# Kernel tuning notes

Measured on AMD Instinct MI355X. Metric: run time of the kernel, lower is better.

Reference implementation:

```python
import jax, jax.numpy as jnp
import numpy as np

B, N, DF, DC = 16, 4096, 128, 3
N_GROUP, K_GROUP = 1024, 16
D_IN, D_OUT = DC + DF, 256  # d_features = [131, 256]
BN_EPS = 1e-5


def farthest_point_sample(coord, n_sample):
    # coord: [B, N, 3] -> idx: [B, n_sample] (deterministic start at point 0)
    b, n, _ = coord.shape
    dist0 = jnp.full((b, n), jnp.inf, coord.dtype)
    idx0 = jnp.zeros((b,), jnp.int32)

    def step(carry, _):
        dist, last = carry
        last_pt = jnp.take_along_axis(coord, last[:, None, None].astype(jnp.int32), axis=1)  # [B,1,3]
        d = jnp.sum((coord - last_pt) ** 2, axis=-1)  # [B,N]
        dist = jnp.minimum(dist, d)
        nxt = jnp.argmax(dist, axis=1).astype(jnp.int32)
        return (dist, nxt), last

    _, idxs = jax.lax.scan(step, (dist0, idx0), None, length=n_sample)
    return jnp.swapaxes(idxs, 0, 1)  # [B, n_sample]


def knn_points(coord, center_coord, k):
    # squared distances [B, G, N]; k nearest source points per center
    d2 = jnp.sum((center_coord[:, :, None, :] - coord[:, None, :, :]) ** 2, axis=-1)
    _, idx = jax.lax.top_k(-d2, k)  # [B, G, k]
    return idx.astype(jnp.int32)


def index_points(points, idx):
    # points: [B, N, C]; idx: [B, ...] -> [B, ..., C]
    b = points.shape[0]
    batch_idx = jnp.arange(b).reshape((b,) + (1,) * (idx.ndim - 1))
    return points[batch_idx, idx]


def setup_inputs() -> dict:
    key = jax.random.key(0)
    k1, k2, k3, k4 = jax.random.split(key, 4)
    feature = jax.random.normal(k1, (B, N, DF), dtype=jnp.float32)
    coord = jax.random.normal(k2, (B, N, DC), dtype=jnp.float32)
    W = jax.random.normal(k3, (D_OUT, D_IN), dtype=jnp.float32) * (1.0 / np.sqrt(D_IN))
    b = jax.random.normal(k4, (D_OUT,), dtype=jnp.float32) * 0.01
    gamma = jnp.ones((D_OUT,), dtype=jnp.float32)
    beta = jnp.zeros((D_OUT,), dtype=jnp.float32)
    return {"feature": feature, "coord": coord, "W": W, "b": b, "gamma": gamma, "beta": beta}


def reference(feature, coord, W, b, gamma, beta):
    # --- group ---
    center_idx = farthest_point_sample(coord, N_GROUP)            # [B,G]
    center_coord = index_points(coord, center_idx)                 # [B,G,3]
    neigh_idx = knn_points(coord, center_coord, K_GROUP)           # [B,G,K]
    neigh_coord = index_points(coord, neigh_idx) - center_coord[:, :, None]  # [B,G,K,3]
    neigh_feature = jnp.concatenate([neigh_coord, index_points(feature, neigh_idx)], axis=-1)  # [B,G,K,131]
    # --- 1x1 conv + BatchNorm (train-mode batch stats, biased var) + ReLU ---
    y = jnp.einsum('bgkc,oc->bgko', neigh_feature, W) + b          # [B,G,K,256]
    mean = jnp.mean(y, axis=(0, 1, 2))
    var = jnp.mean((y - mean) ** 2, axis=(0, 1, 2))
    y = (y - mean) * jax.lax.rsqrt(var + BN_EPS) * gamma + beta
    y = jax.nn.relu(y)
    # --- max over neighbors ---
    center_feature = jnp.max(y, axis=2)                            # [B,G,256]
    return center_feature, center_coord
```

## Files before the change

### kernel.cpp

```cpp
#include <hip/hip_runtime.h>
#include <stdint.h>

#define BATCH 16
#define NPTS 4096
#define DFEAT 128
#define NGRP 1024
#define KNNK 16
#define DOUT_CH 256
#define KPAD 160
#define APAD 168
#define NGROUPS (BATCH*NGRP)
#define MROWS (NGROUPS*KNNK)
#define NWORKERS 240
#define NCHUNKS (NGROUPS/8)
#define CHUNKS_PER_BATCH (NGRP/8)
#define OUT_FEAT_ELEMS (NGROUPS*DOUT_CH)
#define KNN_SLOTS 512
#define PROG_STRIDE 16

typedef __attribute__((ext_vector_type(8))) short s16x8;
typedef __attribute__((ext_vector_type(8))) __bf16 bf16x8;
typedef __attribute__((ext_vector_type(4))) float f32x4;

union V8U { s16x8 s; bf16x8 b; };

__device__ inline unsigned short f2bf(float f) {
  unsigned u = __float_as_uint(f);
  unsigned r = 0x7FFFu + ((u >> 16) & 1u);
  return (unsigned short)((u + r) >> 16);
}

__device__ inline float sqdist3(float ax, float ay, float az,
                                float bx, float by, float bz) {
  float dx = __fsub_rn(ax, bx);
  float dy = __fsub_rn(ay, by);
  float dz = __fsub_rn(az, bz);
  return __fadd_rn(__fadd_rn(__fmul_rn(dx, dx), __fmul_rn(dy, dy)), __fmul_rn(dz, dz));
}

__device__ inline unsigned long long u64max(unsigned long long a, unsigned long long b) {
  return a > b ? a : b;
}

template<int CTRL>
__device__ inline unsigned long long dpp_max_step(unsigned long long k) {
  unsigned hi = (unsigned)(k >> 32), lo = (unsigned)k;
  unsigned hi2 = (unsigned)__builtin_amdgcn_update_dpp(0, (int)hi, CTRL, 0xF, 0xF, true);
  unsigned lo2 = (unsigned)__builtin_amdgcn_update_dpp(0, (int)lo, CTRL, 0xF, 0xF, true);
  unsigned long long k2 = ((unsigned long long)hi2 << 32) | lo2;
  return k2 > k ? k2 : k;
}
__device__ inline unsigned long long wave_max_u64(unsigned long long k) {
  k = dpp_max_step<0xB1>(k);
  k = dpp_max_step<0x4E>(k);
  k = dpp_max_step<0x141>(k);
  k = dpp_max_step<0x140>(k);
  k = dpp_max_step<0x142>(k);
  k = dpp_max_step<0x143>(k);
  return k;
}

template<int CTRL>
__device__ inline unsigned long long dpp_min_step(unsigned long long k) {
  unsigned hi = (unsigned)(k >> 32), lo = (unsigned)k;
  unsigned hi2 = (unsigned)__builtin_amdgcn_update_dpp((int)hi, (int)hi, CTRL, 0xF, 0xF, false);
  unsigned lo2 = (unsigned)__builtin_amdgcn_update_dpp((int)lo, (int)lo, CTRL, 0xF, 0xF, false);
  unsigned long long k2 = ((unsigned long long)hi2 << 32) | lo2;
  return k2 < k ? k2 : k;
}
__device__ inline unsigned long long wave_min_u64(unsigned long long k) {
  k = dpp_min_step<0xB1>(k);
  k = dpp_min_step<0x4E>(k);
  k = dpp_min_step<0x141>(k);
  k = dpp_min_step<0x140>(k);
  k = dpp_min_step<0x142>(k);
  k = dpp_min_step<0x143>(k);
  return k;
}

struct FpsSh {
  float4 c4[NPTS];
  float ocb[NGRP * 3];
  unsigned long long slots[2][4];
};
struct WrkSh {
  float wd[4][NPTS];
  float svd[4][KNN_SLOTS];
  int   svi[4][KNN_SLOTS];
  unsigned short Abuf[2][16][APAD];
  int   nidx_s[8][KNNK];
  float cent_s[8][3];
};
union ShU { FpsSh f; WrkSh w; };

__global__ __launch_bounds__(256)
void fused_kernel(const float* __restrict__ feat, const float* __restrict__ coord,
                  const float* __restrict__ W, float* __restrict__ out_coord,
                  unsigned short* __restrict__ Wb,
                  float* __restrict__ psum, float* __restrict__ psumsq,
                  float* __restrict__ wmax, float* __restrict__ wmin,
                  int* __restrict__ progress, int* __restrict__ wb_ready)
{
  __shared__ ShU sh;
  const int tid = threadIdx.x;
  const int w = tid >> 6;
  const int lane = tid & 63;

  if (blockIdx.x < BATCH) {
    const int b = blockIdx.x;
    float4* c4 = sh.f.c4;
    float* ocb = sh.f.ocb;

    const float* g = coord + (size_t)b * NPTS * 3;
    for (int p = tid; p < NPTS; p += 256)
      c4[p] = make_float4(g[3 * p], g[3 * p + 1], g[3 * p + 2], 0.f);
    __syncthreads();

    float px[16], py[16], pz[16], dist[16];
    unsigned lokey[16];
    #pragma unroll
    for (int j = 0; j < 16; ++j) {
      int p = tid + 256 * j;
      float4 c = c4[p];
      px[j] = c.x; py[j] = c.y; pz[j] = c.z;
      dist[j] = __builtin_inff();
      lokey[j] = 0xFFFFFFFFu - (unsigned)p;
    }

    float lx = c4[0].x, ly = c4[0].y, lz = c4[0].z;
    if (tid == 0) { ocb[0] = lx; ocb[1] = ly; ocb[2] = lz; }

    float* oc = out_coord + (size_t)b * NGRP * 3;
    int pend = 0;

    for (int i = 1; i < NGRP; ++i) {
      const int par = i & 1;
      unsigned long long cand[16];
      #pragma unroll
      for (int j = 0; j < 16; ++j) {
        float d  = sqdist3(px[j], py[j], pz[j], lx, ly, lz);
        float nd = fminf(dist[j], d);
        dist[j] = nd;
        cand[j] = ((unsigned long long)__float_as_uint(nd) << 32) | lokey[j];
      }
      #pragma unroll
      for (int st = 8; st >= 1; st >>= 1)
        #pragma unroll
        for (int j = 0; j < st; ++j)
          cand[j] = u64max(cand[j], cand[j + st]);
      unsigned long long best = wave_max_u64(cand[0]);
      if (lane == 63) sh.f.slots[par][w] = best;
      __syncthreads();

      if (pend) {
        if (tid == 0) {
          __threadfence();
          __hip_atomic_store(&progress[b * PROG_STRIDE], pend, __ATOMIC_RELEASE, __HIP_MEMORY_SCOPE_AGENT);
        }
        pend = 0;
      }
      if ((i & 7) == 0) {
        if (tid < 24) oc[(i - 8) * 3 + tid] = ocb[(i - 8) * 3 + tid];
        pend = i;
      }

      unsigned long long s0 = u64max(sh.f.slots[par][0], sh.f.slots[par][1]);
      unsigned long long s1 = u64max(sh.f.slots[par][2], sh.f.slots[par][3]);
      unsigned long long f = u64max(s0, s1);
      int mi = (int)(0xFFFFFFFFu - (unsigned)(f & 0xFFFFFFFFull));

      float4 cw = c4[mi];
      lx = cw.x; ly = cw.y; lz = cw.z;
      if (tid < 3) ocb[3 * i + tid] = (tid == 0) ? cw.x : ((tid == 1) ? cw.y : cw.z);
    }

    __syncthreads();
    #pragma unroll
    for (int qq = 0; qq < 12; ++qq) oc[tid + 256 * qq] = ocb[tid + 256 * qq];
    __syncthreads();
    if (tid == 0) {
      __threadfence();
      __hip_atomic_store(&progress[b * PROG_STRIDE], NGRP, __ATOMIC_RELEASE, __HIP_MEMORY_SCOPE_AGENT);
    }
    return;
  }

  const int wi = blockIdx.x - BATCH;

  if (wi == 0) {
    for (int i = tid; i < DOUT_CH * KPAD; i += 256) {
      int n = i / KPAD;
      int k = i - n * KPAD;
      float v = 0.f;
      if (k < 128)      v = W[n * 131 + 3 + k];
      else if (k < 131) v = W[n * 131 + (k - 128)];
      Wb[i] = f2bf(v);
    }
    __syncthreads();
    if (tid == 0) {
      __threadfence();
      __hip_atomic_store(wb_ready, 1, __ATOMIC_RELEASE, __HIP_MEMORY_SCOPE_AGENT);
    }
  }
  if (tid == 0) {
    while (__hip_atomic_load(wb_ready, __ATOMIC_RELAXED, __HIP_MEMORY_SCOPE_AGENT) == 0)
      __builtin_amdgcn_s_sleep(1);
    __threadfence();
  }
  __syncthreads();

  const int lr = lane & 15, q = lane >> 4;

  V8U bfrag[4][5];
  #pragma unroll
  for (int nt = 0; nt < 4; ++nt)
    #pragma unroll
    for (int kt = 0; kt < 5; ++kt) {
      int n = w * 64 + nt * 16 + lr;
      bfrag[nt][kt].s = *(const s16x8*)(Wb + n * KPAD + kt * 32 + q * 8);
    }

  for (int i = tid; i < 2 * 16 * 32; i += 256) {
    int buf = i >> 9, rr = (i >> 5) & 15, cc = 128 + (i & 31);
    sh.w.Abuf[buf][rr][cc] = 0;
  }
  float sum1[4] = {0, 0, 0, 0}, sum2[4] = {0, 0, 0, 0};
  __syncthreads();

  for (int ord = wi; ord < NCHUNKS; ord += NWORKERS) {
    const int b  = ord & 15;
    const int lc = ord >> 4;
    const int need = lc * 8 + 8;

    if (tid == 0) {
      while (__hip_atomic_load(&progress[b * PROG_STRIDE], __ATOMIC_RELAXED, __HIP_MEMORY_SCOPE_AGENT) < need)
        __builtin_amdgcn_s_sleep(16);
      __threadfence();
    }
    __syncthreads();

    if (tid < 24) sh.w.cent_s[tid / 3][tid % 3] =
        out_coord[(size_t)b * NGRP * 3 + lc * 24 + tid];
    __syncthreads();

    const float* pc = coord + (size_t)b * NPTS * 3;
    for (int k2 = 0; k2 < 2; ++k2) {
      const int k8 = w * 2 + k2;
      const float cx = sh.w.cent_s[k8][0], cy = sh.w.cent_s[k8][1], cz = sh.w.cent_s[k8][2];
      float* wd  = sh.w.wd[w];
      float* wsd = sh.w.svd[w];
      int*   wsi = sh.w.svi[w];

      float m = __builtin_inff();
      for (int tt = 0; tt < 64; ++tt) {
        int p = tt * 64 + lane;
        float d = sqdist3(cx, cy, cz, pc[3 * p], pc[3 * p + 1], pc[3 * p + 2]);
        wd[p] = d;
        m = fminf(m, d);
      }
      unsigned mb = __float_as_uint(m);
      unsigned prefix = 0u;
      for (int bit = 30; bit >= 0; --bit) {
        unsigned trial = prefix | (1u << bit);
        if (__popcll(__ballot(mb < trial)) < 16) prefix = trial;
      }
      const unsigned T = prefix;

      int base = 0;
      unsigned long long ltmask = (1ull << lane) - 1ull;
      for (int tt = 0; tt < 64; ++tt) {
        int p = tt * 64 + lane;
        float d = wd[p];
        bool keep = (__float_as_uint(d) <= T);
        unsigned long long mk = __ballot(keep);
        if (keep) {
          int pos = base + __popcll(mk & ltmask);
          if (pos < KNN_SLOTS) { wsd[pos] = d; wsi[pos] = p; }
        }
        base += __popcll(mk);
      }
      int S = base < KNN_SLOTS ? base : KNN_SLOTS;

      float rsd[8];
      #pragma unroll
      for (int k = 0; k < 8; ++k) {
        int s = lane + 64 * k;
        rsd[k] = (s < S) ? wsd[s] : __builtin_inff();
      }
      for (int r = 0; r < KNNK; ++r) {
        unsigned long long key = 0xFFFFFFFFFFFFFFFFull;
        #pragma unroll
        for (int k = 0; k < 8; ++k) {
          unsigned long long kk = ((unsigned long long)__float_as_uint(rsd[k]) << 32)
                                | (unsigned)(lane + 64 * k);
          key = kk < key ? kk : key;
        }
        key = wave_min_u64(key);
        int bs = __builtin_amdgcn_readlane((int)(unsigned)(key & 0xFFFFFFFFull), 63);
        #pragma unroll
        for (int k = 0; k < 8; ++k)
          if (lane == (bs & 63) && k == (bs >> 6)) rsd[k] = __builtin_inff();
        if (lane == 0) sh.w.nidx_s[k8][r] = wsi[bs];
      }
    }
    __syncthreads();

    auto stage = [&](int gi, int buf) {
      int r = tid >> 4, c16 = tid & 15;
      int np = sh.w.nidx_s[gi][r];
      const float* fr = feat + ((size_t)(b * NPTS + np)) * DFEAT + c16 * 8;
      float4 f0 = ((const float4*)fr)[0];
      float4 f1 = ((const float4*)fr)[1];
      s16x8 v;
      v[0] = f2bf(f0.x); v[1] = f2bf(f0.y); v[2] = f2bf(f0.z); v[3] = f2bf(f0.w);
      v[4] = f2bf(f1.x); v[5] = f2bf(f1.y); v[6] = f2bf(f1.z); v[7] = f2bf(f1.w);
      *(s16x8*)&sh.w.Abuf[buf][r][c16 * 8] = v;
      if (tid < 16) {
        int np2 = sh.w.nidx_s[gi][tid];
        const float* p = coord + ((size_t)(b * NPTS + np2)) * 3;
        sh.w.Abuf[buf][tid][128] = f2bf(p[0] - sh.w.cent_s[gi][0]);
        sh.w.Abuf[buf][tid][129] = f2bf(p[1] - sh.w.cent_s[gi][1]);
        sh.w.Abuf[buf][tid][130] = f2bf(p[2] - sh.w.cent_s[gi][2]);
      }
    };

    stage(0, 0);
    __syncthreads();

    for (int gi = 0; gi < 8; ++gi) {
      int cur = gi & 1;
      if (gi < 7) stage(gi + 1, cur ^ 1);

      f32x4 acc[4];
      #pragma unroll
      for (int nt = 0; nt < 4; ++nt) acc[nt] = (f32x4)0.0f;
      #pragma unroll
      for (int kt = 0; kt < 5; ++kt) {
        V8U a;
        a.s = *(const s16x8*)&sh.w.Abuf[cur][lr][kt * 32 + q * 8];
        #pragma unroll
        for (int nt = 0; nt < 4; ++nt)
          acc[nt] = __builtin_amdgcn_mfma_f32_16x16x32_bf16(a.b, bfrag[nt][kt].b, acc[nt], 0, 0, 0);
      }
      int gidx = (b * CHUNKS_PER_BATCH + lc) * 8 + gi;
      #pragma unroll
      for (int nt = 0; nt < 4; ++nt) {
        float r0 = acc[nt][0], r1 = acc[nt][1], r2 = acc[nt][2], r3 = acc[nt][3];
        float mx = fmaxf(fmaxf(r0, r1), fmaxf(r2, r3));
        float mn = fminf(fminf(r0, r1), fminf(r2, r3));
        sum1[nt] += r0 + r1 + r2 + r3;
        sum2[nt] += r0 * r0 + r1 * r1 + r2 * r2 + r3 * r3;
        mx = fmaxf(mx, __shfl_xor(mx, 16)); mn = fminf(mn, __shfl_xor(mn, 16));
        mx = fmaxf(mx, __shfl_xor(mx, 32)); mn = fminf(mn, __shfl_xor(mn, 32));
        if (q == 0) {
          int col = w * 64 + nt * 16 + lr;
          wmax[(size_t)gidx * DOUT_CH + col] = mx;
          wmin[(size_t)gidx * DOUT_CH + col] = mn;
        }
      }
      __syncthreads();
    }
  }

  #pragma unroll
  for (int nt = 0; nt < 4; ++nt) {
    float s1 = sum1[nt], s2 = sum2[nt];
    s1 += __shfl_xor(s1, 16); s2 += __shfl_xor(s2, 16);
    s1 += __shfl_xor(s1, 32); s2 += __shfl_xor(s2, 32);
    if (q == 0) {
      int col = w * 64 + nt * 16 + lr;
      psum[(size_t)col * NWORKERS + wi]   = s1;
      psumsq[(size_t)col * NWORKERS + wi] = s2;
    }
  }
}

__global__ __launch_bounds__(256)
void stats_kernel(const float* __restrict__ psum, const float* __restrict__ psumsq,
                  const float* __restrict__ gamma, const float* __restrict__ beta,
                  float* __restrict__ sc, float* __restrict__ tc)
{
  const int c = blockIdx.x;
  const int tid = threadIdx.x, lane = tid & 63, w = tid >> 6;
  float s1 = 0.f, s2 = 0.f;
  for (int r = tid; r < NWORKERS; r += 256) {
    s1 += psum[(size_t)c * NWORKERS + r];
    s2 += psumsq[(size_t)c * NWORKERS + r];
  }
  #pragma unroll
  for (int off = 1; off < 64; off <<= 1) { s1 += __shfl_xor(s1, off); s2 += __shfl_xor(s2, off); }
  __shared__ float a1[4], a2[4];
  if (lane == 0) { a1[w] = s1; a2[w] = s2; }
  __syncthreads();
  if (tid == 0) {
    float S1 = a1[0] + a1[1] + a1[2] + a1[3];
    float S2 = a2[0] + a2[1] + a2[2] + a2[3];
    const float inv = 1.0f / (float)MROWS;
    float mean = S1 * inv;
    float var  = S2 * inv - mean * mean;
    float rs = rsqrtf(var + 1e-5f);
    float s = gamma[c] * rs;
    sc[c] = s;
    tc[c] = beta[c] - mean * s;
  }
}

__global__ __launch_bounds__(256)
void final_kernel(const float* __restrict__ wmax, const float* __restrict__ wmin,
                  const float* __restrict__ sc, const float* __restrict__ tc,
                  float* __restrict__ out)
{
  int i4 = blockIdx.x * 256 + threadIdx.x;
  int base = i4 * 4;
  int c = base & (DOUT_CH - 1);
  float4 mx = *(const float4*)(wmax + base);
  float4 mn = *(const float4*)(wmin + base);
  float4 sv = *(const float4*)(sc + c);
  float4 tv = *(const float4*)(tc + c);
  float4 o;
  o.x = fmaxf(fmaf(sv.x, (sv.x > 0.f ? mx.x : mn.x), tv.x), 0.f);
  o.y = fmaxf(fmaf(sv.y, (sv.y > 0.f ? mx.y : mn.y), tv.y), 0.f);
  o.z = fmaxf(fmaf(sv.z, (sv.z > 0.f ? mx.z : mn.z), tv.z), 0.f);
  o.w = fmaxf(fmaf(sv.w, (sv.w > 0.f ? mx.w : mn.w), tv.w), 0.f);
  *(float4*)(out + base) = o;
}

extern "C" void kernel_launch(void* const* d_in, const int* in_sizes, int n_in,
                              void* d_out, int out_size, void* d_ws, size_t ws_size,
                              hipStream_t stream)
{
  const float* feature = (const float*)d_in[0];
  const float* coord   = (const float*)d_in[1];
  const float* W       = (const float*)d_in[2];
  const float* gamma   = (const float*)d_in[4];
  const float* beta    = (const float*)d_in[5];
  float* out = (float*)d_out;
  float* out_coord = out + OUT_FEAT_ELEMS;

  char* ws = (char*)d_ws;
  int*            flags  = (int*)(ws + 0);
  unsigned short* Wb     = (unsigned short*)(ws + 4096);
  float*          psum   = (float*)(ws + (1 << 20));
  float*          psumsq = (float*)(ws + (2 << 20));
  float*          sc     = (float*)(ws + (3 << 20));
  float*          tc     = (float*)(ws + (3 << 20) + 4096);
  float*          wmax   = (float*)(ws + (8 << 20));
  float*          wmin   = (float*)(ws + (8 << 20) + (size_t)OUT_FEAT_ELEMS * 4);
  int* progress = flags;
  int* wb_ready = flags + BATCH * PROG_STRIDE;

  hipMemsetAsync(flags, 0, (BATCH * PROG_STRIDE + 16) * sizeof(int), stream);

  hipLaunchKernelGGL(fused_kernel, dim3(BATCH + NWORKERS), dim3(256), 0, stream,
                     feature, coord, W, out_coord, Wb,
                     psum, psumsq, wmax, wmin, progress, wb_ready);
  hipLaunchKernelGGL(stats_kernel, dim3(DOUT_CH), dim3(256), 0, stream,
                     psum, psumsq, gamma, beta, sc, tc);
  hipLaunchKernelGGL(final_kernel, dim3(OUT_FEAT_ELEMS / 1024), dim3(256), 0, stream,
                     wmax, wmin, sc, tc, out);
}
```

Baseline: 799.4 us.

## Pack FPS distance math, batch progress publishes, simplify stats reduction

The farthest-point-sampling loop now computes two points' distances at a time with packed v_pk_add/v_pk_mul f32 instructions, which halves VALU issue on the serial critical path. Center coordinates are published every 32 iterations instead of every 8, and the explicit threadfences before the release stores are dropped. The per-worker BN partial sums move to a worker-major layout so a single-block stats kernel can reduce them with coalesced loads. Less frequent publishing may make consumer blocks wait longer for centers, and removing the fences relies on release semantics alone.

Measured after the change: 855.0 us. 7.0% more time.

```diff
diff --git a/kernel.cpp b/kernel.cpp
--- a/kernel.cpp
+++ b/kernel.cpp
@@ -21,6 +21,7 @@
 typedef __attribute__((ext_vector_type(8))) short s16x8;
 typedef __attribute__((ext_vector_type(8))) __bf16 bf16x8;
 typedef __attribute__((ext_vector_type(4))) float f32x4;
+typedef __attribute__((ext_vector_type(2))) float f32x2;
 
 union V8U { s16x8 s; bf16x8 b; };
 
@@ -36,6 +37,22 @@
   float dy = __fsub_rn(ay, by);
   float dz = __fsub_rn(az, bz);
   return __fadd_rn(__fadd_rn(__fmul_rn(dx, dx), __fmul_rn(dy, dy)), __fmul_rn(dz, dz));
+}
+
+__device__ inline f32x2 pk_sub(f32x2 a, f32x2 b) {
+  f32x2 d;
+  asm("v_pk_add_f32 %0, %1, %2 neg_lo:[0,1] neg_hi:[0,1]" : "=v"(d) : "v"(a), "v"(b));
+  return d;
+}
+__device__ inline f32x2 pk_mul(f32x2 a, f32x2 b) {
+  f32x2 d;
+  asm("v_pk_mul_f32 %0, %1, %2" : "=v"(d) : "v"(a), "v"(b));
+  return d;
+}
+__device__ inline f32x2 pk_add(f32x2 a, f32x2 b) {
+  f32x2 d;
+  asm("v_pk_add_f32 %0, %1, %2" : "=v"(d) : "v"(a), "v"(b));
+  return d;
 }
 
 __device__ inline unsigned long long u64max(unsigned long long a, unsigned long long b) {
@@ -116,15 +133,19 @@
       c4[p] = make_float4(g[3 * p], g[3 * p + 1], g[3 * p + 2], 0.f);
     __syncthreads();
 
-    float px[16], py[16], pz[16], dist[16];
+    f32x2 px2[8], py2[8], pz2[8], dist2[8];
     unsigned lokey[16];
     #pragma unroll
-    for (int j = 0; j < 16; ++j) {
-      int p = tid + 256 * j;
-      float4 c = c4[p];
-      px[j] = c.x; py[j] = c.y; pz[j] = c.z;
-      dist[j] = __builtin_inff();
-      lokey[j] = 0xFFFFFFFFu - (unsigned)p;
+    for (int j = 0; j < 8; ++j) {
+      int p0 = tid + 256 * (2 * j);
+      int p1 = tid + 256 * (2 * j + 1);
+      float4 a = c4[p0], c = c4[p1];
+      px2[j] = (f32x2){a.x, c.x};
+      py2[j] = (f32x2){a.y, c.y};
+      pz2[j] = (f32x2){a.z, c.z};
+      dist2[j] = (f32x2){__builtin_inff(), __builtin_inff()};
+      lokey[2 * j]     = 0xFFFFFFFFu - (unsigned)p0;
+      lokey[2 * j + 1] = 0xFFFFFFFFu - (unsigned)p1;
     }
 
     float lx = c4[0].x, ly = c4[0].y, lz = c4[0].z;
@@ -135,13 +156,22 @@
 
     for (int i = 1; i < NGRP; ++i) {
       const int par = i & 1;
+      f32x2 l2x = (f32x2){lx, lx};
+      f32x2 l2y = (f32x2){ly, ly};
+      f32x2 l2z = (f32x2){lz, lz};
+
       unsigned long long cand[16];
       #pragma unroll
-      for (int j = 0; j < 16; ++j) {
-        float d  = sqdist3(px[j], py[j], pz[j], lx, ly, lz);
-        float nd = fminf(dist[j], d);
-        dist[j] = nd;
-        cand[j] = ((unsigned long long)__float_as_uint(nd) << 32) | lokey[j];
+      for (int j = 0; j < 8; ++j) {
+        f32x2 dx = pk_sub(px2[j], l2x);
+        f32x2 dy = pk_sub(py2[j], l2y);
+        f32x2 dz = pk_sub(pz2[j], l2z);
+        f32x2 s = pk_add(pk_add(pk_mul(dx, dx), pk_mul(dy, dy)), pk_mul(dz, dz));
+        float n0 = fminf(dist2[j].x, s.x);
+        float n1 = fminf(dist2[j].y, s.y);
+        dist2[j] = (f32x2){n0, n1};
+        cand[2 * j]     = ((unsigned long long)__float_as_uint(n0) << 32) | lokey[2 * j];
+        cand[2 * j + 1] = ((unsigned long long)__float_as_uint(n1) << 32) | lokey[2 * j + 1];
       }
       #pragma unroll
       for (int st = 8; st >= 1; st >>= 1)
@@ -153,14 +183,12 @@
       __syncthreads();
 
       if (pend) {
-        if (tid == 0) {
-          __threadfence();
+        if (tid == 0)
           __hip_atomic_store(&progress[b * PROG_STRIDE], pend, __ATOMIC_RELEASE, __HIP_MEMORY_SCOPE_AGENT);
-        }
         pend = 0;
       }
-      if ((i & 7) == 0) {
-        if (tid < 24) oc[(i - 8) * 3 + tid] = ocb[(i - 8) * 3 + tid];
+      if ((i & 31) == 0) {
+        if (tid < 96) oc[(i - 32) * 3 + tid] = ocb[(i - 32) * 3 + tid];
         pend = i;
       }
 
@@ -178,10 +206,8 @@
     #pragma unroll
     for (int qq = 0; qq < 12; ++qq) oc[tid + 256 * qq] = ocb[tid + 256 * qq];
     __syncthreads();
-    if (tid == 0) {
-      __threadfence();
+    if (tid == 0)
       __hip_atomic_store(&progress[b * PROG_STRIDE], NGRP, __ATOMIC_RELEASE, __HIP_MEMORY_SCOPE_AGENT);
-    }
     return;
   }
 
@@ -197,10 +223,8 @@
       Wb[i] = f2bf(v);
     }
     __syncthreads();
-    if (tid == 0) {
-      __threadfence();
+    if (tid == 0)
       __hip_atomic_store(wb_ready, 1, __ATOMIC_RELEASE, __HIP_MEMORY_SCOPE_AGENT);
-    }
   }
   if (tid == 0) {
     while (__hip_atomic_load(wb_ready, __ATOMIC_RELAXED, __HIP_MEMORY_SCOPE_AGENT) == 0)
@@ -369,8 +393,8 @@
     s1 += __shfl_xor(s1, 32); s2 += __shfl_xor(s2, 32);
     if (q == 0) {
       int col = w * 64 + nt * 16 + lr;
-      psum[(size_t)col * NWORKERS + wi]   = s1;
-      psumsq[(size_t)col * NWORKERS + wi] = s2;
+      psum[wi * DOUT_CH + col]   = s1;
+      psumsq[wi * DOUT_CH + col] = s2;
     }
   }
 }
@@ -380,29 +404,19 @@
                   const float* __restrict__ gamma, const float* __restrict__ beta,
                   float* __restrict__ sc, float* __restrict__ tc)
 {
-  const int c = blockIdx.x;
-  const int tid = threadIdx.x, lane = tid & 63, w = tid >> 6;
+  const int c = threadIdx.x;
   float s1 = 0.f, s2 = 0.f;
-  for (int r = tid; r < NWORKERS; r += 256) {
-    s1 += psum[(size_t)c * NWORKERS + r];
-    s2 += psumsq[(size_t)c * NWORKERS + r];
-  }
-  #pragma unroll
-  for (int off = 1; off < 64; off <<= 1) { s1 += __shfl_xor(s1, off); s2 += __shfl_xor(s2, off); }
-  __shared__ float a1[4], a2[4];
-  if (lane == 0) { a1[w] = s1; a2[w] = s2; }
-  __syncthreads();
-  if (tid == 0) {
-    float S1 = a1[0] + a1[1] + a1[2] + a1[3];
-    float S2 = a2[0] + a2[1] + a2[2] + a2[3];
-    const float inv = 1.0f / (float)MROWS;
-    float mean = S1 * inv;
-    float var  = S2 * inv - mean * mean;
-    float rs = rsqrtf(var + 1e-5f);
-    float s = gamma[c] * rs;
-    sc[c] = s;
-    tc[c] = beta[c] - mean * s;
-  }
+  for (int r = 0; r < NWORKERS; ++r) {
+    s1 += psum[r * DOUT_CH + c];
+    s2 += psumsq[r * DOUT_CH + c];
+  }
+  const float inv = 1.0f / (float)MROWS;
+  float mean = s1 * inv;
+  float var  = s2 * inv - mean * mean;
+  float rs = rsqrtf(var + 1e-5f);
+  float s = gamma[c] * rs;
+  sc[c] = s;
+  tc[c] = beta[c] - mean * s;
 }
 
 __global__ __launch_bounds__(256)
@@ -449,12 +463,12 @@
   int* progress = flags;
   int* wb_ready = flags + BATCH * PROG_STRIDE;
 
-  hipMemsetAsync(flags, 0, (BATCH * PROG_STRIDE + 16) * sizeof(int), stream);
+  hipMemsetAsync(flags, 0, 2048, stream);
 
   hipLaunchKernelGGL(fused_kernel, dim3(BATCH + NWORKERS), dim3(256), 0, stream,
                      feature, coord, W, out_coord, Wb,
                      psum, psumsq, wmax, wmin, progress, wb_ready);
-  hipLaunchKernelGGL(stats_kernel, dim3(DOUT_CH), dim3(256), 0, stream,
+  hipLaunchKernelGGL(stats_kernel, dim3(1), dim3(256), 0, stream,
                      psum, psumsq, gamma, beta, sc, tc);
   hipLaunchKernelGGL(final_kernel, dim3(OUT_FEAT_ELEMS / 1024), dim3(256), 0, stream,
                      wmax, wmin, sc, tc, out);
```

## Batch FPS progress publishing, drop redundant fences, transpose partial-stat layout

Applied to the files above, without the earlier changes.

The FPS producer now publishes progress to consumer workers every 32 centers instead of every 8 and drops the explicit __threadfence before release atomic stores, which cuts global-memory synchronisation on the serial critical path. Partial BN sums are stored worker-major so writes and the stats-kernel reads are coalesced, and the stats kernel shrinks to one wave with no shared-memory reduction. The coarser publishing means consumers may wait longer for the first groups. Removing the fences relies on release semantics alone for visibility.

New measurement: 813.0 us. No clear change (+1.7%).

```diff
diff --git a/kernel.cpp b/kernel.cpp
--- a/kernel.cpp
+++ b/kernel.cpp
@@ -153,14 +153,12 @@
       __syncthreads();
 
       if (pend) {
-        if (tid == 0) {
-          __threadfence();
+        if (tid == 0)
           __hip_atomic_store(&progress[b * PROG_STRIDE], pend, __ATOMIC_RELEASE, __HIP_MEMORY_SCOPE_AGENT);
-        }
         pend = 0;
       }
-      if ((i & 7) == 0) {
-        if (tid < 24) oc[(i - 8) * 3 + tid] = ocb[(i - 8) * 3 + tid];
+      if ((i & 31) == 0) {
+        if (tid < 96) oc[(i - 32) * 3 + tid] = ocb[(i - 32) * 3 + tid];
         pend = i;
       }
 
@@ -178,10 +176,8 @@
     #pragma unroll
     for (int qq = 0; qq < 12; ++qq) oc[tid + 256 * qq] = ocb[tid + 256 * qq];
     __syncthreads();
-    if (tid == 0) {
-      __threadfence();
+    if (tid == 0)
       __hip_atomic_store(&progress[b * PROG_STRIDE], NGRP, __ATOMIC_RELEASE, __HIP_MEMORY_SCOPE_AGENT);
-    }
     return;
   }
 
@@ -197,10 +193,8 @@
       Wb[i] = f2bf(v);
     }
     __syncthreads();
-    if (tid == 0) {
-      __threadfence();
+    if (tid == 0)
       __hip_atomic_store(wb_ready, 1, __ATOMIC_RELEASE, __HIP_MEMORY_SCOPE_AGENT);
-    }
   }
   if (tid == 0) {
     while (__hip_atomic_load(wb_ready, __ATOMIC_RELAXED, __HIP_MEMORY_SCOPE_AGENT) == 0)
@@ -369,35 +363,30 @@
     s1 += __shfl_xor(s1, 32); s2 += __shfl_xor(s2, 32);
     if (q == 0) {
       int col = w * 64 + nt * 16 + lr;
-      psum[(size_t)col * NWORKERS + wi]   = s1;
-      psumsq[(size_t)col * NWORKERS + wi] = s2;
-    }
-  }
-}
-
-__global__ __launch_bounds__(256)
+      psum[wi * DOUT_CH + col]   = s1;
+      psumsq[wi * DOUT_CH + col] = s2;
+    }
+  }
+}
+
+__global__ __launch_bounds__(64)
 void stats_kernel(const float* __restrict__ psum, const float* __restrict__ psumsq,
                   const float* __restrict__ gamma, const float* __restrict__ beta,
                   float* __restrict__ sc, float* __restrict__ tc)
 {
   const int c = blockIdx.x;
-  const int tid = threadIdx.x, lane = tid & 63, w = tid >> 6;
+  const int lane = threadIdx.x;
   float s1 = 0.f, s2 = 0.f;
-  for (int r = tid; r < NWORKERS; r += 256) {
-    s1 += psum[(size_t)c * NWORKERS + r];
-    s2 += psumsq[(size_t)c * NWORKERS + r];
+  for (int r = lane; r < NWORKERS; r += 64) {
+    s1 += psum[r * DOUT_CH + c];
+    s2 += psumsq[r * DOUT_CH + c];
   }
   #pragma unroll
   for (int off = 1; off < 64; off <<= 1) { s1 += __shfl_xor(s1, off); s2 += __shfl_xor(s2, off); }
-  __shared__ float a1[4], a2[4];
-  if (lane == 0) { a1[w] = s1; a2[w] = s2; }
-  __syncthreads();
-  if (tid == 0) {
-    float S1 = a1[0] + a1[1] + a1[2] + a1[3];
-    float S2 = a2[0] + a2[1] + a2[2] + a2[3];
+  if (lane == 0) {
     const float inv = 1.0f / (float)MROWS;
-    float mean = S1 * inv;
-    float var  = S2 * inv - mean * mean;
+    float mean = s1 * inv;
+    float var  = s2 * inv - mean * mean;
     float rs = rsqrtf(var + 1e-5f);
     float s = gamma[c] * rs;
     sc[c] = s;
@@ -449,12 +438,12 @@
   int* progress = flags;
   int* wb_ready = flags + BATCH * PROG_STRIDE;
 
-  hipMemsetAsync(flags, 0, (BATCH * PROG_STRIDE + 16) * sizeof(int), stream);
+  hipMemsetAsync(flags, 0, 2048, stream);
 
   hipLaunchKernelGGL(fused_kernel, dim3(BATCH + NWORKERS), dim3(256), 0, stream,
                      feature, coord, W, out_coord, Wb,
                      psum, psumsq, wmax, wmin, progress, wb_ready);
-  hipLaunchKernelGGL(stats_kernel, dim3(DOUT_CH), dim3(256), 0, stream,
+  hipLaunchKernelGGL(stats_kernel, dim3(DOUT_CH), dim3(64), 0, stream,
                      psum, psumsq, gamma, beta, sc, tc);
   hipLaunchKernelGGL(final_kernel, dim3(OUT_FEAT_ELEMS / 1024), dim3(256), 0, stream,
                      wmax, wmin, sc, tc, out);
```
